# Kernel tuning notes

Measured on AMD Instinct MI355X. Metric: run time of the kernel, lower is better.

## Reference

```python
import jax, jax.numpy as jnp
import numpy as np

B, C, H, W = 8, 512, 32, 32
MID = 64  # in_ch // k = 512 // 8
BN_EPS = 1e-5


def conv1x1(x, Wt, b):
    # x: [B,C,H,W], Wt: [O,C], b: [O]
    return jnp.einsum('bchw,oc->bohw', x, Wt) + b[None, :, None, None]


def batchnorm(x, gamma, beta):
    # train-mode BN: batch statistics over (B,H,W)
    mu = jnp.mean(x, axis=(0, 2, 3), keepdims=True)
    var = jnp.var(x, axis=(0, 2, 3), keepdims=True)
    xn = (x - mu) * jax.lax.rsqrt(var + BN_EPS)
    return xn * gamma[None, :, None, None] + beta[None, :, None, None]


def setup_inputs() -> dict:
    key = jax.random.key(0)
    ks = jax.random.split(key, 8)
    scale = 1.0 / np.sqrt(C)
    x = jax.random.normal(ks[0], (B, C, H, W), dtype=jnp.float32)
    Wf = jax.random.normal(ks[1], (MID, C), dtype=jnp.float32) * scale
    Wg = jax.random.normal(ks[2], (MID, C), dtype=jnp.float32) * scale
    Wh = jax.random.normal(ks[3], (MID, C), dtype=jnp.float32) * scale
    Wv = jax.random.normal(ks[4], (C, MID), dtype=jnp.float32) * (1.0 / np.sqrt(MID))
    return {
        'x': x,
        'Wf': Wf, 'bf': jnp.zeros((MID,), jnp.float32),
        'gamma_f': jnp.ones((MID,), jnp.float32), 'beta_f': jnp.zeros((MID,), jnp.float32),
        'Wg': Wg, 'bg': jnp.zeros((MID,), jnp.float32),
        'gamma_g': jnp.ones((MID,), jnp.float32), 'beta_g': jnp.zeros((MID,), jnp.float32),
        'Wh': Wh, 'bh': jnp.zeros((MID,), jnp.float32),
        'Wv': Wv, 'bv': jnp.zeros((C,), jnp.float32),
    }


def reference(x, Wf, bf, gamma_f, beta_f, Wg, bg, gamma_g, beta_g, Wh, bh, Wv, bv):
    b, c, h, w = x.shape
    hw = h * w
    f_x = jax.nn.relu(batchnorm(conv1x1(x, Wf, bf), gamma_f, beta_f)).reshape(b, MID, hw)
    g_x = jax.nn.relu(batchnorm(conv1x1(x, Wg, bg), gamma_g, beta_g)).reshape(b, MID, hw)
    h_x = conv1x1(x, Wh, bh).reshape(b, MID, hw)
    # z = f_x^T @ g_x : [B, HW, HW]
    z = jnp.einsum('bcn,bcm->bnm', f_x, g_x)
    # spectral normalization by the top singular value
    S = jnp.linalg.svd(z, compute_uv=False)  # sorted descending
    sigma = S[:, 0][:, None, None]
    attn = z / sigma
    # attn @ h_x^T -> [B, HW, MID], then permute to [B, MID, H, W]
    z2 = jnp.einsum('bnm,bcm->bcn', attn, h_x).reshape(b, MID, h, w)
    return conv1x1(z2, Wv, bv) + x
```

## Files before the change

### kernel.cpp

```cpp
#include <hip/hip_runtime.h>

#define B_   8
#define C_   512
#define HW_  1024
#define MID_ 64
#define NCOL (B_*HW_)
#define NROWS 192
#define EPS  1e-5f

#define YOFF  0
#define YSZ   (NROWS*NCOL)
#define SSOFF (YOFF+YSZ)
#define SSSZ  256
#define WOFF  (SSOFF+SSSZ)
#define WSZ   98304
#define CPOFF (WOFF+WSZ)

typedef unsigned short u16;
typedef __attribute__((ext_vector_type(8))) short short8;
typedef __attribute__((ext_vector_type(4))) float f32x4;

__device__ __forceinline__ u16 f2bf(float f) {
  unsigned u = __float_as_uint(f);
  unsigned r = u + 0x7fffu + ((u >> 16) & 1u);
  return (u16)(r >> 16);
}
__device__ __forceinline__ float bf2f(u16 h) {
  return __uint_as_float(((unsigned)h) << 16);
}
#define MFMA_B16(a,b,c) __builtin_amdgcn_mfma_f32_16x16x32_bf16(a,b,c,0,0,0)

__global__ __launch_bounds__(256) void k_prep(
    const float* __restrict__ Wf, const float* __restrict__ Wg,
    const float* __restrict__ Wh, float* __restrict__ ws)
{
  u16* Whi = (u16*)(ws + WOFF);
  u16* Wlo = Whi + NROWS*C_;
  const int e4 = blockIdx.x*256 + threadIdx.x;
  const int e  = e4*4;
  const int row = e >> 9, k = e & 511;
  const float* src = (row < 64) ? &Wf[row*C_ + k]
                   : (row < 128) ? &Wg[(row-64)*C_ + k]
                   : &Wh[(row-128)*C_ + k];
  const float4 v = *reinterpret_cast<const float4*>(src);
  u16 h0=f2bf(v.x), h1=f2bf(v.y), h2=f2bf(v.z), h3=f2bf(v.w);
  u16 l0=f2bf(v.x-bf2f(h0)), l1=f2bf(v.y-bf2f(h1)), l2=f2bf(v.z-bf2f(h2)), l3=f2bf(v.w-bf2f(h3));
  uint2 ph; ph.x = (unsigned)h0 | ((unsigned)h1<<16); ph.y = (unsigned)h2 | ((unsigned)h3<<16);
  uint2 pl; pl.x = (unsigned)l0 | ((unsigned)l1<<16); pl.y = (unsigned)l2 | ((unsigned)l3<<16);
  *reinterpret_cast<uint2*>(&Whi[e]) = ph;
  *reinterpret_cast<uint2*>(&Wlo[e]) = pl;
}

__global__ __launch_bounds__(256) void k_conv(
    const float* __restrict__ x,
    const float* __restrict__ bf, const float* __restrict__ bg, const float* __restrict__ bh,
    float* __restrict__ ws)
{
  __shared__ u16 Xh[8*32*8];
  __shared__ u16 Xl[8*32*8];
  const u16* Whi = (const u16*)(ws + WOFF);
  const u16* Wlo = Whi + NROWS*C_;
  const int n0  = blockIdx.x * 32;
  const int b   = n0 >> 10;
  const int hw0 = n0 & 1023;
  const int t   = threadIdx.x;
  const int lane = t & 63;
  const int wid  = t >> 6;
  const int wrow0 = wid * 48;
  const int cst  = t & 31;
  const int kg2  = t >> 5;
  const int lm   = lane & 15;
  const int lk   = lane >> 4;

  f32x4 acc[3][2];
  #pragma unroll
  for (int i=0;i<3;++i) { acc[i][0]=(f32x4)0.f; acc[i][1]=(f32x4)0.f; }

  for (int kk = 0; kk < C_; kk += 64) {
    __syncthreads();
    {
      const float* xp = x + ((size_t)(b*C_ + kk + kg2*8))*HW_ + hw0 + cst;
      u16 hb[8], lb[8];
      #pragma unroll
      for (int i=0;i<8;++i) {
        const float v = xp[(size_t)i*HW_];
        hb[i] = f2bf(v); lb[i] = f2bf(v - bf2f(hb[i]));
      }
      uint4 ph, pl;
      ph.x=(unsigned)hb[0]|((unsigned)hb[1]<<16); ph.y=(unsigned)hb[2]|((unsigned)hb[3]<<16);
      ph.z=(unsigned)hb[4]|((unsigned)hb[5]<<16); ph.w=(unsigned)hb[6]|((unsigned)hb[7]<<16);
      pl.x=(unsigned)lb[0]|((unsigned)lb[1]<<16); pl.y=(unsigned)lb[2]|((unsigned)lb[3]<<16);
      pl.z=(unsigned)lb[4]|((unsigned)lb[5]<<16); pl.w=(unsigned)lb[6]|((unsigned)lb[7]<<16);
      *reinterpret_cast<uint4*>(&Xh[(kg2*32+cst)*8]) = ph;
      *reinterpret_cast<uint4*>(&Xl[(kg2*32+cst)*8]) = pl;
    }
    __syncthreads();
    #pragma unroll
    for (int kb = 0; kb < 2; ++kb) {
      short8 bhf[2], blf[2];
      #pragma unroll
      for (int nt = 0; nt < 2; ++nt) {
        const int col = nt*16 + lm;
        const int idx = ((kb*4 + lk)*32 + col)*8;
        bhf[nt] = *reinterpret_cast<const short8*>(&Xh[idx]);
        blf[nt] = *reinterpret_cast<const short8*>(&Xl[idx]);
      }
      #pragma unroll
      for (int mt = 0; mt < 3; ++mt) {
        const int row = wrow0 + mt*16 + lm;
        const size_t widx = (size_t)row*C_ + kk + kb*32 + lk*8;
        const short8 ah = *reinterpret_cast<const short8*>(&Whi[widx]);
        const short8 al = *reinterpret_cast<const short8*>(&Wlo[widx]);
        #pragma unroll
        for (int nt = 0; nt < 2; ++nt) {
          acc[mt][nt] = MFMA_B16(ah, bhf[nt], acc[mt][nt]);
          acc[mt][nt] = MFMA_B16(al, bhf[nt], acc[mt][nt]);
          acc[mt][nt] = MFMA_B16(ah, blf[nt], acc[mt][nt]);
        }
      }
    }
  }
  #pragma unroll
  for (int mt = 0; mt < 3; ++mt) {
    const int rbase = wrow0 + mt*16;
    const float* bp = (rbase < 64) ? bf : (rbase < 128) ? bg : bh;
    const int rloc0 = (rbase & 63) + lk*4;
    #pragma unroll
    for (int nt = 0; nt < 2; ++nt) {
      const int col = n0 + nt*16 + lm;
      #pragma unroll
      for (int r = 0; r < 4; ++r) {
        const int row = rbase + lk*4 + r;
        ws[YOFF + (size_t)row*NCOL + col] = acc[mt][nt][r] + bp[rloc0 + r];
      }
    }
  }
}

__global__ __launch_bounds__(256) void k_stats(
    const float* __restrict__ gamma_f, const float* __restrict__ beta_f,
    const float* __restrict__ gamma_g, const float* __restrict__ beta_g,
    float* __restrict__ ws)
{
  const int r = blockIdx.x;
  const float4* Yr = reinterpret_cast<const float4*>(ws + YOFF + (size_t)r*NCOL);
  const int t = threadIdx.x;
  float s = 0.f, s2 = 0.f;
  for (int n = t; n < NCOL/4; n += 256) {
    const float4 v = Yr[n];
    s  += (v.x+v.y)+(v.z+v.w);
    s2 += (v.x*v.x+v.y*v.y)+(v.z*v.z+v.w*v.w);
  }
  __shared__ float sh[256], sh2[256];
  sh[t] = s; sh2[t] = s2;
  __syncthreads();
  for (int st = 128; st > 0; st >>= 1) {
    if (t < st) { sh[t] += sh[t+st]; sh2[t] += sh2[t+st]; }
    __syncthreads();
  }
  if (t == 0) {
    const float mean = sh[0] * (1.0f/NCOL);
    const float var  = sh2[0] * (1.0f/NCOL) - mean*mean;
    float g, be; int j;
    if (r < 64) { j = r;     g = gamma_f[j]; be = beta_f[j]; }
    else        { j = r-64;  g = gamma_g[j]; be = beta_g[j]; }
    const float sc = g * rsqrtf(var + EPS);
    const float sf = be - mean*sc;
    if (r < 64) { ws[SSOFF + j]       = sc; ws[SSOFF + 64  + j] = sf; }
    else        { ws[SSOFF + 128 + j] = sc; ws[SSOFF + 192 + j] = sf; }
  }
}

__global__ __launch_bounds__(256) void k_cpart(float* __restrict__ ws, int nchunk)
{
  __shared__ u16 Sh[3][64][72];
  __shared__ u16 Sl[3][64][72];
  const int chunk = blockIdx.x, b = blockIdx.y;
  const int chunkcols = 1024 / nchunk;
  const int bcol0 = b*1024 + chunk*chunkcols;
  const float* Y = ws + YOFF;
  const float* SS = ws + SSOFF;
  const int t = threadIdx.x;
  const int lane = t & 63, wid = t >> 6;
  const int lm = lane & 15, lk = lane >> 4;
  const int mt0 = (wid >> 1) * 2;
  const int nt0 = (wid & 1) * 2;

  f32x4 acc[3][2][2];
  #pragma unroll
  for (int p=0;p<3;++p) for (int i=0;i<2;++i) for (int j=0;j<2;++j) acc[p][i][j]=(f32x4)0.f;

  for (int kk = 0; kk < chunkcols; kk += 64) {
    __syncthreads();
    for (int q = t; q < 3072; q += 256) {
      const int mm = q >> 10, rem = q & 1023;
      const int r = rem >> 4, c4 = (rem & 15) * 4;
      const float4 v = *reinterpret_cast<const float4*>(
          &Y[(size_t)(mm*64 + r)*NCOL + bcol0 + kk + c4]);
      float v0, v1, v2, v3;
      if (mm < 2) {
        const float sc = SS[mm*128 + r], sf = SS[mm*128 + 64 + r];
        v0 = fmaxf(sc*v.x+sf, 0.f); v1 = fmaxf(sc*v.y+sf, 0.f);
        v2 = fmaxf(sc*v.z+sf, 0.f); v3 = fmaxf(sc*v.w+sf, 0.f);
      } else { v0=v.x; v1=v.y; v2=v.z; v3=v.w; }
      const u16 h0=f2bf(v0), h1=f2bf(v1), h2=f2bf(v2), h3=f2bf(v3);
      uint2 ph; ph.x=(unsigned)h0|((unsigned)h1<<16); ph.y=(unsigned)h2|((unsigned)h3<<16);
      uint2 pl;
      pl.x=(unsigned)f2bf(v0-bf2f(h0)) | ((unsigned)f2bf(v1-bf2f(h1))<<16);
      pl.y=(unsigned)f2bf(v2-bf2f(h2)) | ((unsigned)f2bf(v3-bf2f(h3))<<16);
      *reinterpret_cast<uint2*>(&Sh[mm][r][c4]) = ph;
      *reinterpret_cast<uint2*>(&Sl[mm][r][c4]) = pl;
    }
    __syncthreads();
    #pragma unroll
    for (int kb = 0; kb < 2; ++kb) {
      const int ko = kb*32 + lk*8;
      short8 ah[3][2], al[3][2];
      #pragma unroll
      for (int m = 0; m < 3; ++m)
        #pragma unroll
        for (int mi = 0; mi < 2; ++mi) {
          const int row = (mt0+mi)*16 + lm;
          ah[m][mi] = *reinterpret_cast<const short8*>(&Sh[m][row][ko]);
          al[m][mi] = *reinterpret_cast<const short8*>(&Sl[m][row][ko]);
        }
      short8 bhf[2][2], blf[2][2];
      #pragma unroll
      for (int m = 0; m < 2; ++m)
        #pragma unroll
        for (int ni = 0; ni < 2; ++ni) {
          const int row = (nt0+ni)*16 + lm;
          bhf[m][ni] = *reinterpret_cast<const short8*>(&Sh[m][row][ko]);
          blf[m][ni] = *reinterpret_cast<const short8*>(&Sl[m][row][ko]);
        }
      #pragma unroll
      for (int p = 0; p < 3; ++p) {
        const int am = p;
        const int bm = (p==0) ? 0 : 1;
        #pragma unroll
        for (int mi = 0; mi < 2; ++mi)
          #pragma unroll
          for (int ni = 0; ni < 2; ++ni) {
            acc[p][mi][ni] = MFMA_B16(ah[am][mi], bhf[bm][ni], acc[p][mi][ni]);
            acc[p][mi][ni] = MFMA_B16(al[am][mi], bhf[bm][ni], acc[p][mi][ni]);
            acc[p][mi][ni] = MFMA_B16(ah[am][mi], blf[bm][ni], acc[p][mi][ni]);
          }
      }
    }
  }
  float* cp = ws + CPOFF;
  #pragma unroll
  for (int p = 0; p < 3; ++p) {
    float* base = cp + ((size_t)((b*3+p)*nchunk + chunk))*4096;
    #pragma unroll
    for (int mi = 0; mi < 2; ++mi)
      #pragma unroll
      for (int ni = 0; ni < 2; ++ni) {
        const int col = (nt0+ni)*16 + lm;
        #pragma unroll
        for (int r = 0; r < 4; ++r) {
          const int row = (mt0+mi)*16 + lk*4 + r;
          base[(size_t)row*64 + col] = acc[p][mi][ni][r];
        }
      }
  }
}

__global__ __launch_bounds__(256) void k_creduce(float* __restrict__ ws, int nchunk)
{
  const int m = blockIdx.y;
  const int q = blockIdx.x*256 + threadIdx.x;
  const float4* src = reinterpret_cast<const float4*>(ws + CPOFF) + (size_t)m*nchunk*1024;
  const size_t cmoff = (size_t)CPOFF + (size_t)B_*3*nchunk*4096;
  float4 s = {0.f,0.f,0.f,0.f};
  for (int ch = 0; ch < nchunk; ++ch) {
    const float4 p = src[(size_t)ch*1024 + q];
    s.x+=p.x; s.y+=p.y; s.z+=p.z; s.w+=p.w;
  }
  *(reinterpret_cast<float4*>(ws + cmoff) + (size_t)m*1024 + q) = s;
}

__global__ __launch_bounds__(64) void k_sigma(float* __restrict__ ws, int nchunk)
{
  const int b = blockIdx.x;
  const int lane = threadIdx.x;
  const size_t cmoff = (size_t)CPOFF + (size_t)B_*3*nchunk*4096;
  const size_t isoff = cmoff + 24*4096;
  const float* Cf = ws + cmoff + (size_t)(b*3+0)*4096;
  const float* Cg = ws + cmoff + (size_t)(b*3+1)*4096;
  __shared__ float vsh[64];
  __shared__ float ush[64];
  float cfr[64], cgr[64];
  #pragma unroll
  for (int k4 = 0; k4 < 16; ++k4) {
    const float4 fa = *reinterpret_cast<const float4*>(&Cf[lane*64 + k4*4]);
    const float4 fc = *reinterpret_cast<const float4*>(&Cg[lane*64 + k4*4]);
    cfr[k4*4+0]=fa.x; cfr[k4*4+1]=fa.y; cfr[k4*4+2]=fa.z; cfr[k4*4+3]=fa.w;
    cgr[k4*4+0]=fc.x; cgr[k4*4+1]=fc.y; cgr[k4*4+2]=fc.z; cgr[k4*4+3]=fc.w;
  }
  float vloc = 0.125f;
  vsh[lane] = vloc;
  __syncthreads();
  float lambda = 0.f;
  #define NIT 20
  for (int it = 0; it <= NIT; ++it) {
    float u0=0.f,u1=0.f,u2=0.f,u3=0.f;
    #pragma unroll
    for (int j4 = 0; j4 < 16; ++j4) {
      const float4 vq = *reinterpret_cast<const float4*>(&vsh[j4*4]);
      u0 += cfr[j4*4+0]*vq.x; u1 += cfr[j4*4+1]*vq.y;
      u2 += cfr[j4*4+2]*vq.z; u3 += cfr[j4*4+3]*vq.w;
    }
    ush[lane] = (u0+u1)+(u2+u3);
    __syncthreads();
    float w0=0.f,w1=0.f,w2=0.f,w3=0.f;
    #pragma unroll
    for (int j4 = 0; j4 < 16; ++j4) {
      const float4 uq = *reinterpret_cast<const float4*>(&ush[j4*4]);
      w0 += cgr[j4*4+0]*uq.x; w1 += cgr[j4*4+1]*uq.y;
      w2 += cgr[j4*4+2]*uq.z; w3 += cgr[j4*4+3]*uq.w;
    }
    const float w = (w0+w1)+(w2+w3);
    if (it == NIT) {
      float num = vloc * w;
      #pragma unroll
      for (int off = 32; off > 0; off >>= 1) num += __shfl_xor(num, off);
      lambda = num;
    } else {
      float n2 = w*w;
      #pragma unroll
      for (int off = 32; off > 0; off >>= 1) n2 += __shfl_xor(n2, off);
      const float rn = rsqrtf(fmaxf(n2, 1e-30f));
      vloc = w * rn;
      vsh[lane] = vloc;
      __syncthreads();
    }
  }
  if (lane == 0) ws[isoff + b] = rsqrtf(fmaxf(lambda, 1e-30f));
}

__global__ __launch_bounds__(256) void k_ufold(const float* __restrict__ Wv,
                                               float* __restrict__ ws, int nchunk)
{
  __shared__ float Wt[64][64];
  __shared__ float Tl[64][64];
  const int rt = blockIdx.x, b = blockIdx.y;
  const size_t cmoff = (size_t)CPOFF + (size_t)B_*3*nchunk*4096;
  const size_t isoff = cmoff + 24*4096;
  const size_t uoff  = isoff + 16;
  const float* T = ws + cmoff + (size_t)(b*3+2)*4096;
  const float isig = ws[isoff + b];
  const int t = threadIdx.x;
  const int ti = t >> 4, tj = t & 15;
  for (int q = t; q < 1024; q += 256)
    *(reinterpret_cast<float4*>(&Tl[0][0]) + q) = *(reinterpret_cast<const float4*>(T) + q);
  for (int q = t; q < 1024; q += 256) {
    const int row = q >> 4;
    const int c4  = (q & 15) * 4;
    const float4 wv = *reinterpret_cast<const float4*>(&Wv[(size_t)(rt*64+row)*64 + c4]);
    Wt[c4+0][row]=wv.x; Wt[c4+1][row]=wv.y; Wt[c4+2][row]=wv.z; Wt[c4+3][row]=wv.w;
  }
  __syncthreads();
  float acc[4][4] = {};
  #pragma unroll
  for (int c = 0; c < 64; ++c) {
    const float4 a  = *reinterpret_cast<const float4*>(&Wt[c][ti*4]);
    const float4 bb = *reinterpret_cast<const float4*>(&Tl[c][tj*4]);
    acc[0][0]+=a.x*bb.x; acc[0][1]+=a.x*bb.y; acc[0][2]+=a.x*bb.z; acc[0][3]+=a.x*bb.w;
    acc[1][0]+=a.y*bb.x; acc[1][1]+=a.y*bb.y; acc[1][2]+=a.y*bb.z; acc[1][3]+=a.y*bb.w;
    acc[2][0]+=a.z*bb.x; acc[2][1]+=a.z*bb.y; acc[2][2]+=a.z*bb.z; acc[2][3]+=a.z*bb.w;
    acc[3][0]+=a.w*bb.x; acc[3][1]+=a.w*bb.y; acc[3][2]+=a.w*bb.z; acc[3][3]+=a.w*bb.w;
  }
  #pragma unroll
  for (int i = 0; i < 4; ++i) {
    float4 o; o.x = acc[i][0]*isig; o.y = acc[i][1]*isig; o.z = acc[i][2]*isig; o.w = acc[i][3]*isig;
    *reinterpret_cast<float4*>(&ws[uoff + ((size_t)b*512 + rt*64 + ti*4+i)*64 + tj*4]) = o;
  }
}

__global__ __launch_bounds__(256) void k_final(
    const float* __restrict__ x, const float* __restrict__ bv,
    float* __restrict__ out, const float* __restrict__ ws, int nchunk)
{
  __shared__ float Ut[64][64];
  __shared__ float Fl[64][64];
  const int nt = blockIdx.x, ot = blockIdx.y, b = blockIdx.z;
  const size_t uoff = (size_t)CPOFF + (size_t)B_*3*nchunk*4096 + 24*4096 + 16;
  const float* scF = ws + SSOFF; const float* sfF = ws + SSOFF + 64;
  const int t = threadIdx.x;
  const int ti = t >> 4, tj = t & 15;
  for (int q = t; q < 1024; q += 256) {
    const int row = q >> 4;
    const int k4  = (q & 15) * 4;
    const float4 uv = *reinterpret_cast<const float4*>(
        &ws[uoff + ((size_t)b*512 + ot*64 + row)*64 + k4]);
    Ut[k4+0][row]=uv.x; Ut[k4+1][row]=uv.y; Ut[k4+2][row]=uv.z; Ut[k4+3][row]=uv.w;
  }
  for (int q = t; q < 1024; q += 256) {
    const int k  = q >> 4;
    const int c4 = (q & 15) * 4;
    const float4 yv = *reinterpret_cast<const float4*>(
        &ws[YOFF + (size_t)k*NCOL + b*1024 + nt*64 + c4]);
    const float s = scF[k], f = sfF[k];
    Fl[k][c4+0]=fmaxf(s*yv.x+f,0.f); Fl[k][c4+1]=fmaxf(s*yv.y+f,0.f);
    Fl[k][c4+2]=fmaxf(s*yv.z+f,0.f); Fl[k][c4+3]=fmaxf(s*yv.w+f,0.f);
  }
  __syncthreads();
  float acc[4][4] = {};
  #pragma unroll
  for (int k = 0; k < 64; ++k) {
    const float4 a  = *reinterpret_cast<const float4*>(&Ut[k][ti*4]);
    const float4 bb = *reinterpret_cast<const float4*>(&Fl[k][tj*4]);
    acc[0][0]+=a.x*bb.x; acc[0][1]+=a.x*bb.y; acc[0][2]+=a.x*bb.z; acc[0][3]+=a.x*bb.w;
    acc[1][0]+=a.y*bb.x; acc[1][1]+=a.y*bb.y; acc[1][2]+=a.y*bb.z; acc[1][3]+=a.y*bb.w;
    acc[2][0]+=a.z*bb.x; acc[2][1]+=a.z*bb.y; acc[2][2]+=a.z*bb.z; acc[2][3]+=a.z*bb.w;
    acc[3][0]+=a.w*bb.x; acc[3][1]+=a.w*bb.y; acc[3][2]+=a.w*bb.z; acc[3][3]+=a.w*bb.w;
  }
  #pragma unroll
  for (int i = 0; i < 4; ++i) {
    const int oc = ot*64 + ti*4 + i;
    const float bvv = bv[oc];
    const size_t base = ((size_t)b*C_ + oc)*HW_ + nt*64 + tj*4;
    const float4 xv = *reinterpret_cast<const float4*>(&x[base]);
    float4 o;
    o.x = acc[i][0]+bvv+xv.x; o.y = acc[i][1]+bvv+xv.y;
    o.z = acc[i][2]+bvv+xv.z; o.w = acc[i][3]+bvv+xv.w;
    *reinterpret_cast<float4*>(&out[base]) = o;
  }
}

extern "C" void kernel_launch(void* const* d_in, const int* in_sizes, int n_in,
                              void* d_out, int out_size, void* d_ws, size_t ws_size,
                              hipStream_t stream) {
  (void)in_sizes; (void)n_in; (void)out_size;
  const float* x       = (const float*)d_in[0];
  const float* Wf      = (const float*)d_in[1];
  const float* bf      = (const float*)d_in[2];
  const float* gamma_f = (const float*)d_in[3];
  const float* beta_f  = (const float*)d_in[4];
  const float* Wg      = (const float*)d_in[5];
  const float* bg      = (const float*)d_in[6];
  const float* gamma_g = (const float*)d_in[7];
  const float* beta_g  = (const float*)d_in[8];
  const float* Wh      = (const float*)d_in[9];
  const float* bh      = (const float*)d_in[10];
  const float* Wv      = (const float*)d_in[11];
  const float* bv      = (const float*)d_in[12];
  float* out = (float*)d_out;
  float* ws  = (float*)d_ws;

  auto need = [](int nc) -> size_t {
    return ((size_t)CPOFF + (size_t)B_*3*nc*4096 + 24*4096 + 16 + (size_t)B_*512*64) * 4;
  };
  const int nchunk = (ws_size >= need(16)) ? 16 : (ws_size >= need(8)) ? 8 : 4;

  k_prep   <<<96,             256, 0, stream>>>(Wf, Wg, Wh, ws);
  k_conv   <<<256,            256, 0, stream>>>(x, bf, bg, bh, ws);
  k_stats  <<<128,            256, 0, stream>>>(gamma_f, beta_f, gamma_g, beta_g, ws);
  k_cpart  <<<dim3(nchunk,8), 256, 0, stream>>>(ws, nchunk);
  k_creduce<<<dim3(4,24),     256, 0, stream>>>(ws, nchunk);
  k_sigma  <<<8,               64, 0, stream>>>(ws, nchunk);
  k_ufold  <<<dim3(8,8),      256, 0, stream>>>(Wv, ws, nchunk);
  k_final  <<<dim3(16,8,8),   256, 0, stream>>>(x, bv, out, ws, nchunk);
}
```

Measured before the change: 92.85 us.

## Fuse BN stats into conv epilogue and merge sigma with U-fold kernel

```diff
diff --git a/kernel.cpp b/kernel.cpp
--- a/kernel.cpp
+++ b/kernel.cpp
@@ -3,18 +3,23 @@
 #define B_   8
 #define C_   512
 #define HW_  1024
-#define MID_ 64
 #define NCOL (B_*HW_)
 #define NROWS 192
 #define EPS  1e-5f
-
-#define YOFF  0
-#define YSZ   (NROWS*NCOL)
-#define SSOFF (YOFF+YSZ)
-#define SSSZ  256
-#define WOFF  (SSOFF+SSSZ)
-#define WSZ   98304
-#define CPOFF (WOFF+WSZ)
+#define NCHUNK 32
+
+#define YOFF   0
+#define YSZ    (NROWS*NCOL)
+#define SPOFF  (YOFF+YSZ)
+#define SPSZ   256
+#define WOFF   (SPOFF+SPSZ)
+#define WSZ    98304
+#define CPOFF  (WOFF+WSZ)
+#define CPSZ   (24*NCHUNK*4096)
+#define CMOFF  (CPOFF+CPSZ)
+#define CMSZ   (24*4096)
+#define ISOFF  (CMOFF+CMSZ)
+#define UOFF   (ISOFF+16)
 
 typedef unsigned short u16;
 typedef __attribute__((ext_vector_type(8))) short short8;
@@ -30,10 +35,17 @@
 }
 #define MFMA_B16(a,b,c) __builtin_amdgcn_mfma_f32_16x16x32_bf16(a,b,c,0,0,0)
 
+#define FMA16(a, bb) \
+  acc[0][0]+=a.x*bb.x; acc[0][1]+=a.x*bb.y; acc[0][2]+=a.x*bb.z; acc[0][3]+=a.x*bb.w; \
+  acc[1][0]+=a.y*bb.x; acc[1][1]+=a.y*bb.y; acc[1][2]+=a.y*bb.z; acc[1][3]+=a.y*bb.w; \
+  acc[2][0]+=a.z*bb.x; acc[2][1]+=a.z*bb.y; acc[2][2]+=a.z*bb.z; acc[2][3]+=a.z*bb.w; \
+  acc[3][0]+=a.w*bb.x; acc[3][1]+=a.w*bb.y; acc[3][2]+=a.w*bb.z; acc[3][3]+=a.w*bb.w;
+
 __global__ __launch_bounds__(256) void k_prep(
     const float* __restrict__ Wf, const float* __restrict__ Wg,
     const float* __restrict__ Wh, float* __restrict__ ws)
 {
+  if (blockIdx.x == 0) ws[SPOFF + threadIdx.x] = 0.f;
   u16* Whi = (u16*)(ws + WOFF);
   u16* Wlo = Whi + NROWS*C_;
   const int e4 = blockIdx.x*256 + threadIdx.x;
@@ -67,10 +79,8 @@
   const int lane = t & 63;
   const int wid  = t >> 6;
   const int wrow0 = wid * 48;
-  const int cst  = t & 31;
-  const int kg2  = t >> 5;
-  const int lm   = lane & 15;
-  const int lk   = lane >> 4;
+  const int cst = t & 31, kg2 = t >> 5;
+  const int lm = lane & 15, lk = lane >> 4;
 
   f32x4 acc[3][2];
   #pragma unroll
@@ -126,295 +136,289 @@
     const float* bp = (rbase < 64) ? bf : (rbase < 128) ? bg : bh;
     const int rloc0 = (rbase & 63) + lk*4;
     #pragma unroll
-    for (int nt = 0; nt < 2; ++nt) {
-      const int col = n0 + nt*16 + lm;
-      #pragma unroll
-      for (int r = 0; r < 4; ++r) {
-        const int row = rbase + lk*4 + r;
-        ws[YOFF + (size_t)row*NCOL + col] = acc[mt][nt][r] + bp[rloc0 + r];
-      }
-    }
-  }
-}
-
-__global__ __launch_bounds__(256) void k_stats(
+    for (int r = 0; r < 4; ++r) {
+      const int row = rbase + lk*4 + r;
+      const float bi = bp[rloc0 + r];
+      const float y0 = acc[mt][0][r] + bi;
+      const float y1 = acc[mt][1][r] + bi;
+      ws[YOFF + (size_t)row*NCOL + n0 + lm]      = y0;
+      ws[YOFF + (size_t)row*NCOL + n0 + 16 + lm] = y1;
+      if (rbase < 128) {
+        float s  = y0 + y1;
+        float s2 = y0*y0 + y1*y1;
+        #pragma unroll
+        for (int off = 1; off < 16; off <<= 1) {
+          s  += __shfl_xor(s,  off);
+          s2 += __shfl_xor(s2, off);
+        }
+        if (lm == 0) {
+          atomicAdd(&ws[SPOFF + row*2 + 0], s);
+          atomicAdd(&ws[SPOFF + row*2 + 1], s2);
+        }
+      }
+    }
+  }
+}
+
+__global__ __launch_bounds__(256) void k_cpart(
     const float* __restrict__ gamma_f, const float* __restrict__ beta_f,
     const float* __restrict__ gamma_g, const float* __restrict__ beta_g,
     float* __restrict__ ws)
 {
-  const int r = blockIdx.x;
-  const float4* Yr = reinterpret_cast<const float4*>(ws + YOFF + (size_t)r*NCOL);
+  __shared__ u16 Sh[3][64][40];
+  __shared__ u16 Sl[3][64][40];
+  __shared__ float scs[128], sfs[128];
+  const int chunk = blockIdx.x, b = blockIdx.y;
   const int t = threadIdx.x;
-  float s = 0.f, s2 = 0.f;
-  for (int n = t; n < NCOL/4; n += 256) {
-    const float4 v = Yr[n];
-    s  += (v.x+v.y)+(v.z+v.w);
-    s2 += (v.x*v.x+v.y*v.y)+(v.z*v.z+v.w*v.w);
-  }
-  __shared__ float sh[256], sh2[256];
-  sh[t] = s; sh2[t] = s2;
+  if (t < 128) {
+    const float s  = ws[SPOFF + t*2 + 0];
+    const float s2 = ws[SPOFF + t*2 + 1];
+    const float mean = s*(1.0f/NCOL);
+    const float var  = s2*(1.0f/NCOL) - mean*mean;
+    const float g  = (t < 64) ? gamma_f[t] : gamma_g[t-64];
+    const float be = (t < 64) ? beta_f[t]  : beta_g[t-64];
+    const float sc = g * rsqrtf(var + EPS);
+    scs[t] = sc; sfs[t] = be - mean*sc;
+  }
   __syncthreads();
-  for (int st = 128; st > 0; st >>= 1) {
-    if (t < st) { sh[t] += sh[t+st]; sh2[t] += sh2[t+st]; }
-    __syncthreads();
-  }
-  if (t == 0) {
-    const float mean = sh[0] * (1.0f/NCOL);
-    const float var  = sh2[0] * (1.0f/NCOL) - mean*mean;
-    float g, be; int j;
-    if (r < 64) { j = r;     g = gamma_f[j]; be = beta_f[j]; }
-    else        { j = r-64;  g = gamma_g[j]; be = beta_g[j]; }
-    const float sc = g * rsqrtf(var + EPS);
-    const float sf = be - mean*sc;
-    if (r < 64) { ws[SSOFF + j]       = sc; ws[SSOFF + 64  + j] = sf; }
-    else        { ws[SSOFF + 128 + j] = sc; ws[SSOFF + 192 + j] = sf; }
-  }
-}
-
-__global__ __launch_bounds__(256) void k_cpart(float* __restrict__ ws, int nchunk)
-{
-  __shared__ u16 Sh[3][64][72];
-  __shared__ u16 Sl[3][64][72];
-  const int chunk = blockIdx.x, b = blockIdx.y;
-  const int chunkcols = 1024 / nchunk;
-  const int bcol0 = b*1024 + chunk*chunkcols;
-  const float* Y = ws + YOFF;
-  const float* SS = ws + SSOFF;
-  const int t = threadIdx.x;
-  const int lane = t & 63, wid = t >> 6;
-  const int lm = lane & 15, lk = lane >> 4;
-  const int mt0 = (wid >> 1) * 2;
-  const int nt0 = (wid & 1) * 2;
-
-  f32x4 acc[3][2][2];
-  #pragma unroll
-  for (int p=0;p<3;++p) for (int i=0;i<2;++i) for (int j=0;j<2;++j) acc[p][i][j]=(f32x4)0.f;
-
-  for (int kk = 0; kk < chunkcols; kk += 64) {
-    __syncthreads();
-    for (int q = t; q < 3072; q += 256) {
-      const int mm = q >> 10, rem = q & 1023;
-      const int r = rem >> 4, c4 = (rem & 15) * 4;
-      const float4 v = *reinterpret_cast<const float4*>(
-          &Y[(size_t)(mm*64 + r)*NCOL + bcol0 + kk + c4]);
-      float v0, v1, v2, v3;
-      if (mm < 2) {
-        const float sc = SS[mm*128 + r], sf = SS[mm*128 + 64 + r];
-        v0 = fmaxf(sc*v.x+sf, 0.f); v1 = fmaxf(sc*v.y+sf, 0.f);
-        v2 = fmaxf(sc*v.z+sf, 0.f); v3 = fmaxf(sc*v.w+sf, 0.f);
-      } else { v0=v.x; v1=v.y; v2=v.z; v3=v.w; }
-      const u16 h0=f2bf(v0), h1=f2bf(v1), h2=f2bf(v2), h3=f2bf(v3);
-      uint2 ph; ph.x=(unsigned)h0|((unsigned)h1<<16); ph.y=(unsigned)h2|((unsigned)h3<<16);
-      uint2 pl;
-      pl.x=(unsigned)f2bf(v0-bf2f(h0)) | ((unsigned)f2bf(v1-bf2f(h1))<<16);
-      pl.y=(unsigned)f2bf(v2-bf2f(h2)) | ((unsigned)f2bf(v3-bf2f(h3))<<16);
-      *reinterpret_cast<uint2*>(&Sh[mm][r][c4]) = ph;
-      *reinterpret_cast<uint2*>(&Sl[mm][r][c4]) = pl;
-    }
-    __syncthreads();
-    #pragma unroll
-    for (int kb = 0; kb < 2; ++kb) {
-      const int ko = kb*32 + lk*8;
-      short8 ah[3][2], al[3][2];
-      #pragma unroll
-      for (int m = 0; m < 3; ++m)
-        #pragma unroll
-        for (int mi = 0; mi < 2; ++mi) {
-          const int row = (mt0+mi)*16 + lm;
-          ah[m][mi] = *reinterpret_cast<const short8*>(&Sh[m][row][ko]);
-          al[m][mi] = *reinterpret_cast<const short8*>(&Sl[m][row][ko]);
-        }
-      short8 bhf[2][2], blf[2][2];
-      #pragma unroll
-      for (int m = 0; m < 2; ++m)
+  const int bcol0 = b*1024 + chunk*32;
+  for (int q = t; q < 1536; q += 256) {
+    const int mm = q >> 9, rem = q & 511;
+    const int r = rem >> 3, c4 = (rem & 7) * 4;
+    const float4 v = *reinterpret_cast<const float4*>(
+        &ws[YOFF + (size_t)(mm*64 + r)*NCOL + bcol0 + c4]);
+    float v0, v1, v2, v3;
+    if (mm < 2) {
+      const float sc = scs[mm*64 + r], sf = sfs[mm*64 + r];
+      v0 = fmaxf(sc*v.x+sf, 0.f); v1 = fmaxf(sc*v.y+sf, 0.f);
+      v2 = fmaxf(sc*v.z+sf, 0.f); v3 = fmaxf(sc*v.w+sf, 0.f);
+    } else { v0=v.x; v1=v.y; v2=v.z; v3=v.w; }
+    const u16 h0=f2bf(v0), h1=f2bf(v1), h2=f2bf(v2), h3=f2bf(v3);
+    uint2 ph; ph.x=(unsigned)h0|((unsigned)h1<<16); ph.y=(unsigned)h2|((unsigned)h3<<16);
+    uint2 pl;
+    pl.x=(unsigned)f2bf(v0-bf2f(h0)) | ((unsigned)f2bf(v1-bf2f(h1))<<16);
+    pl.y=(unsigned)f2bf(v2-bf2f(h2)) | ((unsigned)f2bf(v3-bf2f(h3))<<16);
+    *reinterpret_cast<uint2*>(&Sh[mm][r][c4]) = ph;
+    *reinterpret_cast<uint2*>(&Sl[mm][r][c4]) = pl;
+  }
+  __syncthreads();
+  {
+    const int lane = t & 63, wid = t >> 6;
+    const int lm = lane & 15, lk = lane >> 4;
+    const int mt0 = (wid >> 1)*2, nt0 = (wid & 1)*2;
+    const int ko = lk*8;
+    short8 ah[3][2], al[3][2];
+    #pragma unroll
+    for (int m = 0; m < 3; ++m)
+      #pragma unroll
+      for (int mi = 0; mi < 2; ++mi) {
+        const int row = (mt0+mi)*16 + lm;
+        ah[m][mi] = *reinterpret_cast<const short8*>(&Sh[m][row][ko]);
+        al[m][mi] = *reinterpret_cast<const short8*>(&Sl[m][row][ko]);
+      }
+    short8 bhf[2][2], blf[2][2];
+    #pragma unroll
+    for (int m = 0; m < 2; ++m)
+      #pragma unroll
+      for (int ni = 0; ni < 2; ++ni) {
+        const int row = (nt0+ni)*16 + lm;
+        bhf[m][ni] = *reinterpret_cast<const short8*>(&Sh[m][row][ko]);
+        blf[m][ni] = *reinterpret_cast<const short8*>(&Sl[m][row][ko]);
+      }
+    f32x4 acc2[3][2][2];
+    #pragma unroll
+    for (int p=0;p<3;++p) for (int i=0;i<2;++i) for (int j=0;j<2;++j) acc2[p][i][j]=(f32x4)0.f;
+    #pragma unroll
+    for (int p = 0; p < 3; ++p) {
+      const int am = p;
+      const int bm = (p==0) ? 0 : 1;
+      #pragma unroll
+      for (int mi = 0; mi < 2; ++mi)
         #pragma unroll
         for (int ni = 0; ni < 2; ++ni) {
-          const int row = (nt0+ni)*16 + lm;
-          bhf[m][ni] = *reinterpret_cast<const short8*>(&Sh[m][row][ko]);
-          blf[m][ni] = *reinterpret_cast<const short8*>(&Sl[m][row][ko]);
-        }
-      #pragma unroll
-      for (int p = 0; p < 3; ++p) {
-        const int am = p;
-        const int bm = (p==0) ? 0 : 1;
-        #pragma unroll
-        for (int mi = 0; mi < 2; ++mi)
+          acc2[p][mi][ni] = MFMA_B16(ah[am][mi], bhf[bm][ni], acc2[p][mi][ni]);
+          acc2[p][mi][ni] = MFMA_B16(al[am][mi], bhf[bm][ni], acc2[p][mi][ni]);
+          acc2[p][mi][ni] = MFMA_B16(ah[am][mi], blf[bm][ni], acc2[p][mi][ni]);
+        }
+    }
+    float* cp = ws + CPOFF;
+    #pragma unroll
+    for (int p = 0; p < 3; ++p) {
+      float* base = cp + ((size_t)((b*3+p)*NCHUNK + chunk))*4096;
+      #pragma unroll
+      for (int mi = 0; mi < 2; ++mi)
+        #pragma unroll
+        for (int ni = 0; ni < 2; ++ni) {
+          const int col = (nt0+ni)*16 + lm;
           #pragma unroll
-          for (int ni = 0; ni < 2; ++ni) {
-            acc[p][mi][ni] = MFMA_B16(ah[am][mi], bhf[bm][ni], acc[p][mi][ni]);
-            acc[p][mi][ni] = MFMA_B16(al[am][mi], bhf[bm][ni], acc[p][mi][ni]);
-            acc[p][mi][ni] = MFMA_B16(ah[am][mi], blf[bm][ni], acc[p][mi][ni]);
+          for (int r = 0; r < 4; ++r) {
+            const int row = (mt0+mi)*16 + lk*4 + r;
+            base[(size_t)row*64 + col] = acc2[p][mi][ni][r];
           }
-      }
-    }
-  }
-  float* cp = ws + CPOFF;
-  #pragma unroll
-  for (int p = 0; p < 3; ++p) {
-    float* base = cp + ((size_t)((b*3+p)*nchunk + chunk))*4096;
-    #pragma unroll
-    for (int mi = 0; mi < 2; ++mi)
-      #pragma unroll
-      for (int ni = 0; ni < 2; ++ni) {
-        const int col = (nt0+ni)*16 + lm;
-        #pragma unroll
-        for (int r = 0; r < 4; ++r) {
-          const int row = (mt0+mi)*16 + lk*4 + r;
-          base[(size_t)row*64 + col] = acc[p][mi][ni][r];
-        }
-      }
-  }
-}
-
-__global__ __launch_bounds__(256) void k_creduce(float* __restrict__ ws, int nchunk)
+        }
+    }
+  }
+}
+
+__global__ __launch_bounds__(256) void k_creduce(float* __restrict__ ws)
 {
   const int m = blockIdx.y;
   const int q = blockIdx.x*256 + threadIdx.x;
-  const float4* src = reinterpret_cast<const float4*>(ws + CPOFF) + (size_t)m*nchunk*1024;
-  const size_t cmoff = (size_t)CPOFF + (size_t)B_*3*nchunk*4096;
+  const float4* src = reinterpret_cast<const float4*>(ws + CPOFF) + (size_t)m*NCHUNK*1024;
   float4 s = {0.f,0.f,0.f,0.f};
-  for (int ch = 0; ch < nchunk; ++ch) {
+  #pragma unroll 8
+  for (int ch = 0; ch < NCHUNK; ++ch) {
     const float4 p = src[(size_t)ch*1024 + q];
     s.x+=p.x; s.y+=p.y; s.z+=p.z; s.w+=p.w;
   }
-  *(reinterpret_cast<float4*>(ws + cmoff) + (size_t)m*1024 + q) = s;
-}
-
-__global__ __launch_bounds__(64) void k_sigma(float* __restrict__ ws, int nchunk)
-{
-  const int b = blockIdx.x;
-  const int lane = threadIdx.x;
-  const size_t cmoff = (size_t)CPOFF + (size_t)B_*3*nchunk*4096;
-  const size_t isoff = cmoff + 24*4096;
-  const float* Cf = ws + cmoff + (size_t)(b*3+0)*4096;
-  const float* Cg = ws + cmoff + (size_t)(b*3+1)*4096;
-  __shared__ float vsh[64];
-  __shared__ float ush[64];
-  float cfr[64], cgr[64];
-  #pragma unroll
-  for (int k4 = 0; k4 < 16; ++k4) {
-    const float4 fa = *reinterpret_cast<const float4*>(&Cf[lane*64 + k4*4]);
-    const float4 fc = *reinterpret_cast<const float4*>(&Cg[lane*64 + k4*4]);
-    cfr[k4*4+0]=fa.x; cfr[k4*4+1]=fa.y; cfr[k4*4+2]=fa.z; cfr[k4*4+3]=fa.w;
-    cgr[k4*4+0]=fc.x; cgr[k4*4+1]=fc.y; cgr[k4*4+2]=fc.z; cgr[k4*4+3]=fc.w;
-  }
-  float vloc = 0.125f;
-  vsh[lane] = vloc;
-  __syncthreads();
-  float lambda = 0.f;
-  #define NIT 20
-  for (int it = 0; it <= NIT; ++it) {
-    float u0=0.f,u1=0.f,u2=0.f,u3=0.f;
-    #pragma unroll
-    for (int j4 = 0; j4 < 16; ++j4) {
-      const float4 vq = *reinterpret_cast<const float4*>(&vsh[j4*4]);
-      u0 += cfr[j4*4+0]*vq.x; u1 += cfr[j4*4+1]*vq.y;
-      u2 += cfr[j4*4+2]*vq.z; u3 += cfr[j4*4+3]*vq.w;
-    }
-    ush[lane] = (u0+u1)+(u2+u3);
+  *(reinterpret_cast<float4*>(ws + CMOFF) + (size_t)m*1024 + q) = s;
+}
+
+__global__ __launch_bounds__(256) void k_su(const float* __restrict__ Wv, float* __restrict__ ws)
+{
+  __shared__ float smA[64][64];
+  __shared__ float smB[64][64];
+  const int bid = blockIdx.x;
+  const int t = threadIdx.x;
+  if (bid < 64) {
+    const int b = bid >> 3, rt = bid & 7;
+    const float* T = ws + CMOFF + (size_t)(b*3+2)*4096;
+    for (int q = t; q < 1024; q += 256)
+      *(reinterpret_cast<float4*>(&smB[0][0]) + q) = *(reinterpret_cast<const float4*>(T) + q);
+    for (int q = t; q < 1024; q += 256) {
+      const int row = q >> 4;
+      const int c4  = (q & 15) * 4;
+      const float4 wv = *reinterpret_cast<const float4*>(&Wv[(size_t)(rt*64+row)*64 + c4]);
+      smA[c4+0][row]=wv.x; smA[c4+1][row]=wv.y; smA[c4+2][row]=wv.z; smA[c4+3][row]=wv.w;
+    }
     __syncthreads();
-    float w0=0.f,w1=0.f,w2=0.f,w3=0.f;
-    #pragma unroll
-    for (int j4 = 0; j4 < 16; ++j4) {
-      const float4 uq = *reinterpret_cast<const float4*>(&ush[j4*4]);
-      w0 += cgr[j4*4+0]*uq.x; w1 += cgr[j4*4+1]*uq.y;
-      w2 += cgr[j4*4+2]*uq.z; w3 += cgr[j4*4+3]*uq.w;
-    }
-    const float w = (w0+w1)+(w2+w3);
-    if (it == NIT) {
-      float num = vloc * w;
-      #pragma unroll
-      for (int off = 32; off > 0; off >>= 1) num += __shfl_xor(num, off);
-      lambda = num;
-    } else {
-      float n2 = w*w;
-      #pragma unroll
-      for (int off = 32; off > 0; off >>= 1) n2 += __shfl_xor(n2, off);
-      const float rn = rsqrtf(fmaxf(n2, 1e-30f));
-      vloc = w * rn;
-      vsh[lane] = vloc;
+    const int ti = t >> 4, tj = t & 15;
+    float acc[4][4] = {};
+    #pragma unroll
+    for (int c = 0; c < 64; ++c) {
+      const float4 a  = *reinterpret_cast<const float4*>(&smA[c][ti*4]);
+      const float4 bb = *reinterpret_cast<const float4*>(&smB[c][tj*4]);
+      FMA16(a, bb)
+    }
+    #pragma unroll
+    for (int i = 0; i < 4; ++i) {
+      float4 o; o.x = acc[i][0]; o.y = acc[i][1]; o.z = acc[i][2]; o.w = acc[i][3];
+      *reinterpret_cast<float4*>(&ws[UOFF + ((size_t)b*512 + rt*64 + ti*4+i)*64 + tj*4]) = o;
+    }
+  } else {
+    const int b = bid - 64;
+    float* vsh = &smA[0][0];
+    float* ush = &smA[1][0];
+    const float* Cf = ws + CMOFF + (size_t)(b*3+0)*4096;
+    const float* Cg = ws + CMOFF + (size_t)(b*3+1)*4096;
+    float cfr[64], cgr[64];
+    if (t < 64) {
+      #pragma unroll
+      for (int k4 = 0; k4 < 16; ++k4) {
+        const float4 fa = *reinterpret_cast<const float4*>(&Cf[t*64 + k4*4]);
+        const float4 fc = *reinterpret_cast<const float4*>(&Cg[t*64 + k4*4]);
+        cfr[k4*4+0]=fa.x; cfr[k4*4+1]=fa.y; cfr[k4*4+2]=fa.z; cfr[k4*4+3]=fa.w;
+        cgr[k4*4+0]=fc.x; cgr[k4*4+1]=fc.y; cgr[k4*4+2]=fc.z; cgr[k4*4+3]=fc.w;
+      }
+    }
+    float vloc = 0.125f;
+    if (t < 64) vsh[t] = vloc;
+    __syncthreads();
+    const int NIT = 16;
+    float lambda = 0.f;
+    for (int it = 0; it <= NIT; ++it) {
+      if (t < 64) {
+        float u0=0.f,u1=0.f,u2=0.f,u3=0.f;
+        #pragma unroll
+        for (int j4 = 0; j4 < 16; ++j4) {
+          const float4 vq = *reinterpret_cast<const float4*>(&vsh[j4*4]);
+          u0 += cfr[j4*4+0]*vq.x; u1 += cfr[j4*4+1]*vq.y;
+          u2 += cfr[j4*4+2]*vq.z; u3 += cfr[j4*4+3]*vq.w;
+        }
+        ush[t] = (u0+u1)+(u2+u3);
+      }
       __syncthreads();
-    }
-  }
-  if (lane == 0) ws[isoff + b] = rsqrtf(fmaxf(lambda, 1e-30f));
-}
-
-__global__ __launch_bounds__(256) void k_ufold(const float* __restrict__ Wv,
-                                               float* __restrict__ ws, int nchunk)
-{
-  __shared__ float Wt[64][64];
-  __shared__ float Tl[64][64];
-  const int rt = blockIdx.x, b = blockIdx.y;
-  const size_t cmoff = (size_t)CPOFF + (size_t)B_*3*nchunk*4096;
-  const size_t isoff = cmoff + 24*4096;
-  const size_t uoff  = isoff + 16;
-  const float* T = ws + cmoff + (size_t)(b*3+2)*4096;
-  const float isig = ws[isoff + b];
-  const int t = threadIdx.x;
-  const int ti = t >> 4, tj = t & 15;
-  for (int q = t; q < 1024; q += 256)
-    *(reinterpret_cast<float4*>(&Tl[0][0]) + q) = *(reinterpret_cast<const float4*>(T) + q);
-  for (int q = t; q < 1024; q += 256) {
-    const int row = q >> 4;
-    const int c4  = (q & 15) * 4;
-    const float4 wv = *reinterpret_cast<const float4*>(&Wv[(size_t)(rt*64+row)*64 + c4]);
-    Wt[c4+0][row]=wv.x; Wt[c4+1][row]=wv.y; Wt[c4+2][row]=wv.z; Wt[c4+3][row]=wv.w;
-  }
-  __syncthreads();
-  float acc[4][4] = {};
-  #pragma unroll
-  for (int c = 0; c < 64; ++c) {
-    const float4 a  = *reinterpret_cast<const float4*>(&Wt[c][ti*4]);
-    const float4 bb = *reinterpret_cast<const float4*>(&Tl[c][tj*4]);
-    acc[0][0]+=a.x*bb.x; acc[0][1]+=a.x*bb.y; acc[0][2]+=a.x*bb.z; acc[0][3]+=a.x*bb.w;
-    acc[1][0]+=a.y*bb.x; acc[1][1]+=a.y*bb.y; acc[1][2]+=a.y*bb.z; acc[1][3]+=a.y*bb.w;
-    acc[2][0]+=a.z*bb.x; acc[2][1]+=a.z*bb.y; acc[2][2]+=a.z*bb.z; acc[2][3]+=a.z*bb.w;
-    acc[3][0]+=a.w*bb.x; acc[3][1]+=a.w*bb.y; acc[3][2]+=a.w*bb.z; acc[3][3]+=a.w*bb.w;
-  }
-  #pragma unroll
-  for (int i = 0; i < 4; ++i) {
-    float4 o; o.x = acc[i][0]*isig; o.y = acc[i][1]*isig; o.z = acc[i][2]*isig; o.w = acc[i][3]*isig;
-    *reinterpret_cast<float4*>(&ws[uoff + ((size_t)b*512 + rt*64 + ti*4+i)*64 + tj*4]) = o;
+      float w = 0.f;
+      if (t < 64) {
+        float w0=0.f,w1=0.f,w2=0.f,w3=0.f;
+        #pragma unroll
+        for (int j4 = 0; j4 < 16; ++j4) {
+          const float4 uq = *reinterpret_cast<const float4*>(&ush[j4*4]);
+          w0 += cgr[j4*4+0]*uq.x; w1 += cgr[j4*4+1]*uq.y;
+          w2 += cgr[j4*4+2]*uq.z; w3 += cgr[j4*4+3]*uq.w;
+        }
+        w = (w0+w1)+(w2+w3);
+      }
+      if (it == NIT) {
+        if (t < 64) {
+          float num = vloc * w;
+          #pragma unroll
+          for (int off = 32; off > 0; off >>= 1) num += __shfl_xor(num, off);
+          lambda = num;
+        }
+      } else {
+        if (t < 64) {
+          float n2 = w*w;
+          #pragma unroll
+          for (int off = 32; off > 0; off >>= 1) n2 += __shfl_xor(n2, off);
+          const float rn = rsqrtf(fmaxf(n2, 1e-30f));
+          vloc = w * rn;
+        }
+        __syncthreads();
+        if (t < 64) vsh[t] = vloc;
+        __syncthreads();
+      }
+    }
+    if (t == 0) ws[ISOFF + b] = rsqrtf(fmaxf(lambda, 1e-30f));
   }
 }
 
 __global__ __launch_bounds__(256) void k_final(
     const float* __restrict__ x, const float* __restrict__ bv,
-    float* __restrict__ out, const float* __restrict__ ws, int nchunk)
+    const float* __restrict__ gamma_f, const float* __restrict__ beta_f,
+    float* __restrict__ out, const float* __restrict__ ws)
 {
   __shared__ float Ut[64][64];
   __shared__ float Fl[64][64];
+  __shared__ float scF[64], sfF[64];
   const int nt = blockIdx.x, ot = blockIdx.y, b = blockIdx.z;
-  const size_t uoff = (size_t)CPOFF + (size_t)B_*3*nchunk*4096 + 24*4096 + 16;
-  const float* scF = ws + SSOFF; const float* sfF = ws + SSOFF + 64;
   const int t = threadIdx.x;
-  const int ti = t >> 4, tj = t & 15;
+  if (t < 64) {
+    const float s  = ws[SPOFF + t*2 + 0];
+    const float s2 = ws[SPOFF + t*2 + 1];
+    const float mean = s*(1.0f/NCOL);
+    const float var  = s2*(1.0f/NCOL) - mean*mean;
+    const float sc = gamma_f[t] * rsqrtf(var + EPS);
+    scF[t] = sc; sfF[t] = beta_f[t] - mean*sc;
+  }
   for (int q = t; q < 1024; q += 256) {
-    const int row = q >> 4;
-    const int k4  = (q & 15) * 4;
+    const int row = q >> 4, k4 = (q & 15)*4;
     const float4 uv = *reinterpret_cast<const float4*>(
-        &ws[uoff + ((size_t)b*512 + ot*64 + row)*64 + k4]);
+        &ws[UOFF + ((size_t)b*512 + ot*64 + row)*64 + k4]);
     Ut[k4+0][row]=uv.x; Ut[k4+1][row]=uv.y; Ut[k4+2][row]=uv.z; Ut[k4+3][row]=uv.w;
   }
   for (int q = t; q < 1024; q += 256) {
-    const int k  = q >> 4;
-    const int c4 = (q & 15) * 4;
+    const int k = q >> 4, c4 = (q & 15)*4;
     const float4 yv = *reinterpret_cast<const float4*>(
         &ws[YOFF + (size_t)k*NCOL + b*1024 + nt*64 + c4]);
+    Fl[k][c4+0]=yv.x; Fl[k][c4+1]=yv.y; Fl[k][c4+2]=yv.z; Fl[k][c4+3]=yv.w;
+  }
+  __syncthreads();
+  for (int q = t; q < 1024; q += 256) {
+    const int k = q >> 4, c4 = (q & 15)*4;
     const float s = scF[k], f = sfF[k];
-    Fl[k][c4+0]=fmaxf(s*yv.x+f,0.f); Fl[k][c4+1]=fmaxf(s*yv.y+f,0.f);
-    Fl[k][c4+2]=fmaxf(s*yv.z+f,0.f); Fl[k][c4+3]=fmaxf(s*yv.w+f,0.f);
+    Fl[k][c4+0]=fmaxf(s*Fl[k][c4+0]+f,0.f); Fl[k][c4+1]=fmaxf(s*Fl[k][c4+1]+f,0.f);
+    Fl[k][c4+2]=fmaxf(s*Fl[k][c4+2]+f,0.f); Fl[k][c4+3]=fmaxf(s*Fl[k][c4+3]+f,0.f);
   }
   __syncthreads();
+  const float isig = ws[ISOFF + b];
+  const int ti = t >> 4, tj = t & 15;
   float acc[4][4] = {};
   #pragma unroll
   for (int k = 0; k < 64; ++k) {
     const float4 a  = *reinterpret_cast<const float4*>(&Ut[k][ti*4]);
     const float4 bb = *reinterpret_cast<const float4*>(&Fl[k][tj*4]);
-    acc[0][0]+=a.x*bb.x; acc[0][1]+=a.x*bb.y; acc[0][2]+=a.x*bb.z; acc[0][3]+=a.x*bb.w;
-    acc[1][0]+=a.y*bb.x; acc[1][1]+=a.y*bb.y; acc[1][2]+=a.y*bb.z; acc[1][3]+=a.y*bb.w;
-    acc[2][0]+=a.z*bb.x; acc[2][1]+=a.z*bb.y; acc[2][2]+=a.z*bb.z; acc[2][3]+=a.z*bb.w;
-    acc[3][0]+=a.w*bb.x; acc[3][1]+=a.w*bb.y; acc[3][2]+=a.w*bb.z; acc[3][3]+=a.w*bb.w;
+    FMA16(a, bb)
   }
   #pragma unroll
   for (int i = 0; i < 4; ++i) {
@@ -423,8 +427,8 @@
     const size_t base = ((size_t)b*C_ + oc)*HW_ + nt*64 + tj*4;
     const float4 xv = *reinterpret_cast<const float4*>(&x[base]);
     float4 o;
-    o.x = acc[i][0]+bvv+xv.x; o.y = acc[i][1]+bvv+xv.y;
-    o.z = acc[i][2]+bvv+xv.z; o.w = acc[i][3]+bvv+xv.w;
+    o.x = acc[i][0]*isig+bvv+xv.x; o.y = acc[i][1]*isig+bvv+xv.y;
+    o.z = acc[i][2]*isig+bvv+xv.z; o.w = acc[i][3]*isig+bvv+xv.w;
     *reinterpret_cast<float4*>(&out[base]) = o;
   }
 }
@@ -432,7 +436,7 @@
 extern "C" void kernel_launch(void* const* d_in, const int* in_sizes, int n_in,
                               void* d_out, int out_size, void* d_ws, size_t ws_size,
                               hipStream_t stream) {
-  (void)in_sizes; (void)n_in; (void)out_size;
+  (void)in_sizes; (void)n_in; (void)out_size; (void)ws_size;
   const float* x       = (const float*)d_in[0];
   const float* Wf      = (const float*)d_in[1];
   const float* bf      = (const float*)d_in[2];
@@ -449,17 +453,10 @@
   float* out = (float*)d_out;
   float* ws  = (float*)d_ws;
 
-  auto need = [](int nc) -> size_t {
-    return ((size_t)CPOFF + (size_t)B_*3*nc*4096 + 24*4096 + 16 + (size_t)B_*512*64) * 4;
-  };
-  const int nchunk = (ws_size >= need(16)) ? 16 : (ws_size >= need(8)) ? 8 : 4;
-
-  k_prep   <<<96,             256, 0, stream>>>(Wf, Wg, Wh, ws);
-  k_conv   <<<256,            256, 0, stream>>>(x, bf, bg, bh, ws);
-  k_stats  <<<128,            256, 0, stream>>>(gamma_f, beta_f, gamma_g, beta_g, ws);
-  k_cpart  <<<dim3(nchunk,8), 256, 0, stream>>>(ws, nchunk);
-  k_creduce<<<dim3(4,24),     256, 0, stream>>>(ws, nchunk);
-  k_sigma  <<<8,               64, 0, stream>>>(ws, nchunk);
-  k_ufold  <<<dim3(8,8),      256, 0, stream>>>(Wv, ws, nchunk);
-  k_final  <<<dim3(16,8,8),   256, 0, stream>>>(x, bv, out, ws, nchunk);
-}
+  k_prep   <<<96,              256, 0, stream>>>(Wf, Wg, Wh, ws);
+  k_conv   <<<256,             256, 0, stream>>>(x, bf, bg, bh, ws);
+  k_cpart  <<<dim3(NCHUNK,8),  256, 0, stream>>>(gamma_f, beta_f, gamma_g, beta_g, ws);
+  k_creduce<<<dim3(4,24),      256, 0, stream>>>(ws);
+  k_su     <<<72,              256, 0, stream>>>(Wv, ws);
+  k_final  <<<dim3(16,8,8),    256, 0, stream>>>(x, bv, gamma_f, beta_f, out, ws);
+}
```

After: 139.4 us. 50.1% more time.
